# Kernel optimization log

Measured on AMD Instinct MI355X. Metric: run time of the kernel, lower is better.

## Reference

```python
import jax, jax.numpy as jnp
import numpy as np

BETA = 0.25
DECAY = 0.99
EPS = 1e-05
K = 1024        # num_codebook_vectors
D = 256         # latent_dim


def setup_inputs() -> dict:
    key = jax.random.key(0)
    k1, k2, k3 = jax.random.split(key, 3)
    return {
        "z": jax.random.normal(k1, (32, D, 32, 32), dtype=jnp.float32),
        "embedding": jax.random.normal(k2, (K, D), dtype=jnp.float32),
        "ema_cluster_size": jnp.zeros((K,), dtype=jnp.float32),
        "ema_w": jax.random.normal(k3, (K, D), dtype=jnp.float32),
    }


def reference(z, embedding, ema_cluster_size, ema_w):
    B, C, H, W = z.shape
    zp = jnp.transpose(z, (0, 2, 3, 1))            # [B,H,W,C]
    zf = zp.reshape(-1, C)                          # [N, D], N = B*H*W

    # squared L2 distances: ||z||^2 + ||e||^2 - 2 z e^T  -> [N, K]
    d = (jnp.sum(zf * zf, axis=1, keepdims=True)
         + jnp.sum(embedding * embedding, axis=1)
         - 2.0 * (zf @ embedding.T))
    idx = jnp.argmin(d, axis=1)                     # [N]

    # one-hot @ embedding == gather of codebook rows
    z_q = embedding[idx].reshape(zp.shape)          # [B,H,W,C]

    # EMA codebook update (training branch)
    counts = jnp.zeros((K,), dtype=zf.dtype).at[idx].add(1.0)   # encodings.sum(0)
    cs = ema_cluster_size * DECAY + (1.0 - DECAY) * counts
    n = jnp.sum(cs)
    cs = (cs + EPS) / (n + K * EPS) * n             # Laplace smoothing
    dw = jax.ops.segment_sum(zf, idx, num_segments=K)           # encodings.T @ zf
    new_ema_w = ema_w * DECAY + (1.0 - DECAY) * dw
    new_embedding = new_ema_w / cs[:, None]

    # commitment loss + straight-through estimator
    e_latent_loss = jnp.mean((jax.lax.stop_gradient(z_q) - zp) ** 2)
    loss = BETA * e_latent_loss
    z_q_st = zp + jax.lax.stop_gradient(z_q - zp)
    z_q_out = jnp.transpose(z_q_st, (0, 3, 1, 2))   # [B,C,H,W]

    return z_q_out, idx[:, None], loss, new_embedding, cs, new_ema_w
```

## Files before the change

### kernel.cpp

```cpp
#include <hip/hip_runtime.h>

typedef unsigned long long ull;
typedef __attribute__((ext_vector_type(8))) short bf16x8;
typedef __attribute__((ext_vector_type(4))) float f32x4;
typedef __attribute__((ext_vector_type(8))) unsigned short u16x8;

#define DECAY 0.99f
#define BETA 0.25f
#define EPSV 1e-5f
#define EPSGAP 0.0625f

#define Dd 256
#define Kk 1024
#define Nn 32768
#define ZELEM 8388608

__device__ __forceinline__ unsigned short f2bf(float f) {
    unsigned int x = __float_as_uint(f);
    x += 0x7FFFu + ((x >> 16) & 1u);
    return (unsigned short)(x >> 16);
}
__device__ __forceinline__ float bf2f(unsigned short b) {
    return __uint_as_float(((unsigned int)b) << 16);
}
__device__ __forceinline__ unsigned mono(unsigned b) {
    return b ^ (((int)b >> 31) | 0x80000000u);
}
__device__ __forceinline__ float unmono(unsigned m) {
    unsigned b = (m & 0x80000000u) ? (m ^ 0x80000000u) : ~m;
    return __uint_as_float(b);
}
__device__ __forceinline__ unsigned umin32(unsigned a, unsigned b) { return a < b ? a : b; }
__device__ __forceinline__ unsigned umax32(unsigned a, unsigned b) { return a > b ? a : b; }

__global__ __launch_bounds__(256) void prep_e_kernel(
        const float* __restrict__ emb, unsigned short* __restrict__ ehg,
        unsigned short* __restrict__ elg, float* __restrict__ esq,
        int* __restrict__ hist, int* __restrict__ flagcnt,
        float* __restrict__ loss_fix, float* __restrict__ nsum,
        const float* __restrict__ ema_cs, float* __restrict__ dwr, int nrep) {
    const int nsub = blockIdx.x;
    const int t = threadIdx.x;
    {
        const int per = nrep * 512;
        float4* dst = (float4*)(dwr + (size_t)nsub * per);
        const int n4 = per >> 2;
        for (int j = t; j < n4; j += 256) dst[j] = make_float4(0.f, 0.f, 0.f, 0.f);
    }
    if (nsub < 64) {
        if (t < 16) hist[nsub * 16 + t] = 0;
        if (nsub == 0 && t == 16) flagcnt[0] = 0;
        if (nsub == 0 && t == 17) loss_fix[0] = 0.0f;
        #pragma unroll
        for (int it = 0; it < 2; ++it) {
            const int item = it * 256 + t;
            const int kc = item >> 6, lane = item & 63;
            const int quad = lane >> 4, nl = lane & 15;
            const float* ep = emb + (size_t)(nsub * 16 + nl) * Dd + kc * 32 + quad * 8;
            const float4 a = *(const float4*)ep;
            const float4 b4 = *(const float4*)(ep + 4);
            const float v[8] = {a.x, a.y, a.z, a.w, b4.x, b4.y, b4.z, b4.w};
            u16x8 hi, lo;
            #pragma unroll
            for (int j = 0; j < 8; ++j) {
                const unsigned short h = f2bf(v[j]);
                hi[j] = h;
                lo[j] = f2bf(v[j] - bf2f(h));
            }
            const size_t off = ((size_t)(nsub * 8 + kc) * 64 + lane) * 8;
            *(u16x8*)&ehg[off] = hi;
            *(u16x8*)&elg[off] = lo;
        }
        {
            const int nl = t >> 4, seg = t & 15;
            const float* ep = emb + (size_t)(nsub * 16 + nl) * Dd + seg * 16;
            float s = 0.0f;
            #pragma unroll
            for (int j = 0; j < 4; ++j) {
                const float4 v4 = *(const float4*)(ep + j * 4);
                s += v4.x * v4.x + v4.y * v4.y + v4.z * v4.z + v4.w * v4.w;
            }
            #pragma unroll
            for (int d = 1; d < 16; d <<= 1) s += __shfl_xor(s, d);
            if (seg == 0) esq[nsub * 16 + nl] = s;
        }
    } else if (nsub == 64) {
        __shared__ float wred[4];
        const int w = t >> 6, lane = t & 63;
        float s = ema_cs[t] + ema_cs[t + 256] + ema_cs[t + 512] + ema_cs[t + 768];
        #pragma unroll
        for (int d = 32; d > 0; d >>= 1) s += __shfl_xor(s, d);
        if (lane == 0) wred[w] = s;
        __syncthreads();
        if (t == 0)
            nsum[0] = DECAY * (wred[0] + wred[1] + wred[2] + wred[3])
                      + (1.0f - DECAY) * (float)Nn;
    }
}

__global__ __launch_bounds__(256) void dist_kernel(
        const float* __restrict__ z, const unsigned short* __restrict__ ehg,
        const unsigned short* __restrict__ elg, const float* __restrict__ esq,
        const float* __restrict__ emb,
        float* __restrict__ zq, float* __restrict__ dwr, int repmask,
        int* __restrict__ idx_i, float* __restrict__ idx_f,
        int* __restrict__ hist, int* __restrict__ flagcnt,
        int* __restrict__ flaglist, float* __restrict__ flagval,
        float* __restrict__ loss_p) {
    __shared__ __align__(16) unsigned char smem[70656];
    __shared__ int kidx[64];
    unsigned short* zh = (unsigned short*)smem;
    unsigned short* zl = (unsigned short*)(smem + 32768);
    ull* mb   = (ull*)(smem + 65536);
    ull* ms   = (ull*)(smem + 67584);
    float* zsqp = (float*)(smem + 69632);
    float* eldsf = (float*)smem;

    const int t = threadIdx.x, w = t >> 6, L = t & 63;
    const int quad = L >> 4, lr = L & 15;
    const int m0 = blockIdx.x * 64;
    const int b = m0 >> 10, hw0 = m0 & 1023;

    {
        const int c0 = w * 64;
        const float* zp = z + (size_t)b * 262144 + hw0 + L;
        float s = 0.0f;
        #pragma unroll
        for (int cg = 0; cg < 8; ++cg) {
            float v[8];
            #pragma unroll
            for (int j = 0; j < 8; ++j)
                v[j] = zp[(size_t)(c0 + cg * 8 + j) * 1024];
            u16x8 hi, lo;
            #pragma unroll
            for (int j = 0; j < 8; ++j) {
                s = fmaf(v[j], v[j], s);
                const unsigned short h = f2bf(v[j]);
                hi[j] = h;
                lo[j] = f2bf(v[j] - bf2f(h));
            }
            const int chunk = ((c0 >> 3) + cg) ^ (L & 7);
            *(u16x8*)&zh[L * 256 + chunk * 8] = hi;
            *(u16x8*)&zl[L * 256 + chunk * 8] = lo;
        }
        zsqp[L * 4 + w] = s;
    }
    __syncthreads();

    const unsigned short* ehw = ehg + (size_t)(w * 1024 + L) * 8;
    const unsigned short* elw = elg + (size_t)(w * 1024 + L) * 8;

    unsigned bb[16], ss[16];
    #pragma unroll
    for (int i = 0; i < 16; ++i) { bb[i] = 0xFFFFFFFFu; ss[i] = 0xFFFFFFFFu; }

    bf16x8 Bh[2][2], Bl[2][2];
    #pragma unroll
    for (int ni = 0; ni < 2; ++ni) {
        Bh[0][ni] = *(const bf16x8*)(ehw + (size_t)ni * 4096);
        Bl[0][ni] = *(const bf16x8*)(elw + (size_t)ni * 4096);
    }
    bf16x8 Ah[2][4], Al[2][4];
    #pragma unroll
    for (int mi = 0; mi < 4; ++mi) {
        const int chunk = quad ^ (lr & 7);
        const int o = (mi * 16 + lr) * 256 + chunk * 8;
        Ah[0][mi] = *(const bf16x8*)&zh[o];
        Al[0][mi] = *(const bf16x8*)&zl[o];
    }

    for (int nt = 0; nt < 8; ++nt) {
        f32x4 acc[4][2];
        #pragma unroll
        for (int mi = 0; mi < 4; ++mi)
            #pragma unroll
            for (int ni = 0; ni < 2; ++ni) acc[mi][ni] = (f32x4){0.f, 0.f, 0.f, 0.f};

        #pragma unroll
        for (int kc = 0; kc < 8; ++kc) {
            const int cur = kc & 1, nxt = cur ^ 1;
            const int nkc = (kc + 1) & 7;
            const int nnt = (kc == 7) ? ((nt + 1) & 7) : nt;
            #pragma unroll
            for (int ni = 0; ni < 2; ++ni) {
                const size_t o = (size_t)nnt * 32768 + (size_t)ni * 4096 + (size_t)nkc * 512;
                Bh[nxt][ni] = *(const bf16x8*)(ehw + o);
                Bl[nxt][ni] = *(const bf16x8*)(elw + o);
            }
            #pragma unroll
            for (int mi = 0; mi < 4; ++mi) {
                const int chunk = (nkc * 4 + quad) ^ (lr & 7);
                const int o = (mi * 16 + lr) * 256 + chunk * 8;
                Ah[nxt][mi] = *(const bf16x8*)&zh[o];
                Al[nxt][mi] = *(const bf16x8*)&zl[o];
            }
            __builtin_amdgcn_s_setprio(1);
            #pragma unroll
            for (int mi = 0; mi < 4; ++mi)
                #pragma unroll
                for (int ni = 0; ni < 2; ++ni) {
                    acc[mi][ni] = __builtin_amdgcn_mfma_f32_16x16x32_bf16(Ah[cur][mi], Bh[cur][ni], acc[mi][ni], 0, 0, 0);
                    acc[mi][ni] = __builtin_amdgcn_mfma_f32_16x16x32_bf16(Ah[cur][mi], Bl[cur][ni], acc[mi][ni], 0, 0, 0);
                    acc[mi][ni] = __builtin_amdgcn_mfma_f32_16x16x32_bf16(Al[cur][mi], Bh[cur][ni], acc[mi][ni], 0, 0, 0);
                }
            __builtin_amdgcn_s_setprio(0);
        }
        const int q0 = nt * 8 + w * 2;
        const float e0b = esq[q0 * 16 + lr] + 512.0f;
        const float e1b = esq[(q0 + 1) * 16 + lr] + 512.0f;
        #pragma unroll
        for (int mi = 0; mi < 4; ++mi)
            #pragma unroll
            for (int reg = 0; reg < 4; ++reg) {
                const int i = mi * 4 + reg;
                #pragma unroll
                for (int ni = 0; ni < 2; ++ni) {
                    const float val = fmaf(-2.0f, acc[mi][ni][reg], ni ? e1b : e0b);
                    const unsigned pk = (__float_as_uint(val) & 0xFFFFFFC0u) | (unsigned)(q0 + ni);
                    const unsigned mx = umax32(bb[i], pk);
                    bb[i] = umin32(bb[i], pk);
                    ss[i] = umin32(ss[i], mx);
                }
            }
    }

    #pragma unroll
    for (int mi = 0; mi < 4; ++mi)
        #pragma unroll
        for (int reg = 0; reg < 4; ++reg) {
            const int i = mi * 4 + reg;
            ull b2 = ((ull)(bb[i] & 0xFFFFFFC0u) << 14) | (ull)((bb[i] & 63u) * 16 + lr);
            ull s2 = ((ull)(ss[i] & 0xFFFFFFC0u) << 14) | (ull)((ss[i] & 63u) * 16 + lr);
            #pragma unroll
            for (int d = 1; d < 16; d <<= 1) {
                const ull ob = __shfl_xor(b2, d);
                const ull os = __shfl_xor(s2, d);
                const ull mx = ob < b2 ? b2 : ob;
                b2 = ob < b2 ? ob : b2;
                const ull ns = os < s2 ? os : s2;
                s2 = mx < ns ? mx : ns;
            }
            if (lr == 0) {
                const int row = mi * 16 + quad * 4 + reg;
                mb[w * 64 + row] = b2;
                ms[w * 64 + row] = s2;
            }
        }
    __syncthreads();

    if (t < 64) {
        ull b2 = mb[t], s2 = ms[t];
        #pragma unroll
        for (int ww = 1; ww < 4; ++ww) {
            const ull ob = mb[ww * 64 + t], os = ms[ww * 64 + t];
            const ull mx = ob < b2 ? b2 : ob;
            b2 = ob < b2 ? ob : b2;
            const ull ns = os < s2 ? os : s2;
            s2 = mx < ns ? mx : ns;
        }
        const int k = (int)(b2 & 16383ull);
        const float v1 = __uint_as_float((unsigned)(b2 >> 14)) - 512.0f;
        const float v2 = __uint_as_float((unsigned)(s2 >> 14)) - 512.0f;
        idx_i[m0 + t] = k;
        idx_f[m0 + t] = (float)k;
        kidx[t] = k;
        atomicAdd(&hist[k], 1);
        if (v2 - v1 < EPSGAP) {
            const int pos = atomicAdd(flagcnt, 1);
            flaglist[pos] = m0 + t;
            flagval[pos] = v1;
        }
        float lp = v1 + zsqp[t * 4] + zsqp[t * 4 + 1] + zsqp[t * 4 + 2] + zsqp[t * 4 + 3];
        #pragma unroll
        for (int d = 32; d > 0; d >>= 1) lp += __shfl_down(lp, d);
        if (t == 0) loss_p[blockIdx.x] = lp;
    }
    __syncthreads();

    for (int pr = w; pr < 64; pr += 4) {
        const float* er = emb + (size_t)kidx[pr] * Dd;
        #pragma unroll
        for (int g = 0; g < 4; ++g)
            eldsf[pr * 257 + g * 64 + L] = er[g * 64 + L];
    }
    __syncthreads();

    {
        const int g = t & 15;
        const int cl = t >> 4;
        float* zqb = zq + (size_t)b * 262144 + hw0 + g * 4;
        #pragma unroll
        for (int pass = 0; pass < 16; ++pass) {
            const int c = pass * 16 + cl;
            float4 v;
            v.x = eldsf[(g * 4 + 0) * 257 + c];
            v.y = eldsf[(g * 4 + 1) * 257 + c];
            v.z = eldsf[(g * 4 + 2) * 257 + c];
            v.w = eldsf[(g * 4 + 3) * 257 + c];
            *(float4*)(zqb + (size_t)c * 1024) = v;
        }
    }

    {
        const int c = t;
        const float* zcol = z + (size_t)b * 262144 + (size_t)c * 1024 + hw0;
        float* dwb = dwr + (size_t)(blockIdx.x & repmask) * (Kk * Dd);
        #pragma unroll 4
        for (int p = 0; p < 64; ++p) {
            atomicAdd(&dwb[(size_t)kidx[p] * Dd + c], zcol[p]);
        }
    }
}

__global__ __launch_bounds__(256) void fixup_kernel(
        const float* __restrict__ z, const float* __restrict__ emb,
        const float* __restrict__ esq, const int* __restrict__ flagcnt,
        const int* __restrict__ flaglist, const float* __restrict__ flagval,
        int* __restrict__ idx_i, float* __restrict__ idx_f,
        int* __restrict__ hist, float* __restrict__ loss_fix,
        float* __restrict__ zq, float* __restrict__ dw) {
    __shared__ float zrow[256];
    __shared__ ull red[256];
    __shared__ int s_pair[2];
    const int t = threadIdx.x;
    const int total = flagcnt[0];
    for (int fi = blockIdx.x; fi < total; fi += 512) {
        const int n = flaglist[fi];
        const int b = n >> 10, hw = n & 1023;
        __syncthreads();
        zrow[t] = z[(size_t)b * 262144 + (size_t)t * 1024 + hw];
        __syncthreads();
        ull best = ~0ull;
        #pragma unroll
        for (int kc = 0; kc < 4; ++kc) {
            const int k = t * 4 + kc;
            const float* ep = emb + (size_t)k * Dd;
            float dot = 0.0f;
            #pragma unroll 8
            for (int c4 = 0; c4 < 64; ++c4) {
                const float4 e4 = *(const float4*)(ep + c4 * 4);
                const float4 z4 = *(const float4*)&zrow[c4 * 4];
                dot = fmaf(z4.x, e4.x, dot);
                dot = fmaf(z4.y, e4.y, dot);
                dot = fmaf(z4.z, e4.z, dot);
                dot = fmaf(z4.w, e4.w, dot);
            }
            const float val = esq[k] - 2.0f * dot;
            const ull pk = ((ull)mono(__float_as_uint(val)) << 32) | (unsigned)k;
            if (pk < best) best = pk;
        }
        red[t] = best;
        __syncthreads();
        for (int s = 128; s > 0; s >>= 1) {
            if (t < s) { if (red[t + s] < red[t]) red[t] = red[t + s]; }
            __syncthreads();
        }
        if (t == 0) {
            const int knew = (int)(unsigned)(red[0] & 0xFFFFFFFFull);
            const float vnew = unmono((unsigned)(red[0] >> 32));
            const int kold = idx_i[n];
            s_pair[0] = kold;
            s_pair[1] = knew;
            if (knew != kold) {
                idx_i[n] = knew;
                idx_f[n] = (float)knew;
                atomicSub(&hist[kold], 1);
                atomicAdd(&hist[knew], 1);
            }
            atomicAdd(loss_fix, vnew - flagval[fi]);
        }
        __syncthreads();
        const int kold = s_pair[0], knew = s_pair[1];
        if (knew != kold) {
            const float zv = zrow[t];
            atomicAdd(&dw[(size_t)kold * Dd + t], -zv);
            atomicAdd(&dw[(size_t)knew * Dd + t], zv);
            zq[(size_t)b * 262144 + (size_t)t * 1024 + hw] = emb[(size_t)knew * Dd + t];
        }
    }
}

__global__ __launch_bounds__(256) void finalize2_kernel(
        const float* __restrict__ ema_w, const float* __restrict__ dwr,
        int nrep, const int* __restrict__ hist,
        const float* __restrict__ ema_cs, const float* __restrict__ nsum,
        const float* __restrict__ loss_p, const float* __restrict__ loss_fix,
        float* __restrict__ cs_out, float* __restrict__ loss_out,
        float* __restrict__ new_emb_out, float* __restrict__ new_ema_w_out) {
    const int k = blockIdx.x;
    const int t = threadIdx.x;
    const float n = nsum[0];
    const float csr = ema_cs[k] * DECAY + (1.0f - DECAY) * (float)hist[k];
    const float cs = (csr + EPSV) / (n + (float)Kk * EPSV) * n;
    if (t == 0) cs_out[k] = cs;
    const int i = k * 256 + t;
    float s = 0.0f;
    for (int r = 0; r < nrep; ++r) s += dwr[(size_t)r * (Kk * Dd) + i];
    const float nw = ema_w[i] * DECAY + (1.0f - DECAY) * s;
    new_ema_w_out[i] = nw;
    new_emb_out[i]   = nw / cs;
    if (k == 0) {
        __shared__ float wred[4];
        const int w = t >> 6, lane = t & 63;
        float r2 = loss_p[t] + loss_p[t + 256];
        #pragma unroll
        for (int d = 32; d > 0; d >>= 1) r2 += __shfl_xor(r2, d);
        if (lane == 0) wred[w] = r2;
        __syncthreads();
        if (t == 0)
            loss_out[0] = BETA * (wred[0] + wred[1] + wred[2] + wred[3]
                                  + loss_fix[0]) / (float)ZELEM;
    }
}

extern "C" void kernel_launch(void* const* d_in, const int* in_sizes, int n_in,
                              void* d_out, int out_size, void* d_ws, size_t ws_size,
                              hipStream_t stream) {
    const float* z      = (const float*)d_in[0];
    const float* emb    = (const float*)d_in[1];
    const float* ema_cs = (const float*)d_in[2];
    const float* ema_w  = (const float*)d_in[3];

    float* out = (float*)d_out;
    float* zq_out        = out;
    float* idx_out_f     = out + 8388608;
    float* loss_out      = out + 8421376;
    float* new_emb_out   = out + 8421377;
    float* cs_out        = out + 8683521;
    float* new_ema_w_out = out + 8684545;

    int*   idx_i    = (int*)d_ws;
    int*   flagcnt  = idx_i + 32768;
    float* loss_fix = (float*)(flagcnt + 16);
    int*   flaglist = (int*)(loss_fix + 16);
    float* flagval  = (float*)(flaglist + 32768);
    int*   hist     = (int*)(flagval + 32768);
    float* esq      = (float*)(hist + 1024);
    float* loss_p   = esq + 1024;
    float* nsum     = loss_p + 512;
    unsigned short* ehg = (unsigned short*)(nsum + 16);
    unsigned short* elg = ehg + 262144;
    size_t dwr_off = ((size_t)((char*)(elg + 262144) - (char*)d_ws) + 255) & ~(size_t)255;
    float* dwr = (float*)((char*)d_ws + dwr_off);
    const size_t repbytes = (size_t)Kk * Dd * 4;
    size_t rem = (ws_size > dwr_off) ? ws_size - dwr_off : 0;
    int nrep = 1;
    while (nrep < 8 && (size_t)(nrep * 2) * repbytes <= rem) nrep <<= 1;

    prep_e_kernel<<<512, 256, 0, stream>>>(emb, ehg, elg, esq, hist, flagcnt,
                                           loss_fix, nsum, ema_cs, dwr, nrep);
    dist_kernel<<<Nn / 64, 256, 0, stream>>>(z, ehg, elg, esq, emb, zq_out,
                                             dwr, nrep - 1, idx_i, idx_out_f,
                                             hist, flagcnt, flaglist, flagval,
                                             loss_p);
    fixup_kernel<<<512, 256, 0, stream>>>(z, emb, esq, flagcnt, flaglist,
                                          flagval, idx_i, idx_out_f, hist,
                                          loss_fix, zq_out, dwr);
    finalize2_kernel<<<Kk, 256, 0, stream>>>(ema_w, dwr, nrep, hist, ema_cs,
                                             nsum, loss_p, loss_fix, cs_out,
                                             loss_out, new_emb_out,
                                             new_ema_w_out);
}
```

Before: 231.6 us.

## Track top-3 candidates to split fixup into cheap two-candidate and full rescans

The distance kernel now keeps the three best candidates per row instead of two. Near-tie rows whose third candidate is far enough away go to a new list that the fixup kernel resolves with two exact fp32 dot products. Only rows with a close third candidate still get the full 1024-code rescan. The change aims to cut fixup cost, at the price of extra min/max and shuffle work in the hot distance kernel's per-tile selection and reduction.

```diff
diff --git a/kernel.cpp b/kernel.cpp
--- a/kernel.cpp
+++ b/kernel.cpp
@@ -9,6 +9,7 @@
 #define BETA 0.25f
 #define EPSV 1e-5f
 #define EPSGAP 0.0625f
+#define THR3 0.03125f
 
 #define Dd 256
 #define Kk 1024
@@ -32,6 +33,8 @@
 }
 __device__ __forceinline__ unsigned umin32(unsigned a, unsigned b) { return a < b ? a : b; }
 __device__ __forceinline__ unsigned umax32(unsigned a, unsigned b) { return a > b ? a : b; }
+__device__ __forceinline__ ull umin64(ull a, ull b) { return a < b ? a : b; }
+__device__ __forceinline__ ull umax64(ull a, ull b) { return a > b ? a : b; }
 
 __global__ __launch_bounds__(256) void prep_e_kernel(
         const float* __restrict__ emb, unsigned short* __restrict__ ehg,
@@ -51,6 +54,7 @@
         if (t < 16) hist[nsub * 16 + t] = 0;
         if (nsub == 0 && t == 16) flagcnt[0] = 0;
         if (nsub == 0 && t == 17) loss_fix[0] = 0.0f;
+        if (nsub == 0 && t == 18) flagcnt[1] = 0;
         #pragma unroll
         for (int it = 0; it < 2; ++it) {
             const int item = it * 256 + t;
@@ -105,15 +109,17 @@
         float* __restrict__ zq, float* __restrict__ dwr, int repmask,
         int* __restrict__ idx_i, float* __restrict__ idx_f,
         int* __restrict__ hist, int* __restrict__ flagcnt,
-        int* __restrict__ flaglist, float* __restrict__ flagval,
-        float* __restrict__ loss_p) {
-    __shared__ __align__(16) unsigned char smem[70656];
+        int* __restrict__ listA, int* __restrict__ kkA,
+        float* __restrict__ valA, int* __restrict__ listB,
+        float* __restrict__ valB, float* __restrict__ loss_p) {
+    __shared__ __align__(16) unsigned char smem[72704];
     __shared__ int kidx[64];
     unsigned short* zh = (unsigned short*)smem;
     unsigned short* zl = (unsigned short*)(smem + 32768);
     ull* mb   = (ull*)(smem + 65536);
     ull* ms   = (ull*)(smem + 67584);
     float* zsqp = (float*)(smem + 69632);
+    ull* mt   = (ull*)(smem + 70656);
     float* eldsf = (float*)smem;
 
     const int t = threadIdx.x, w = t >> 6, L = t & 63;
@@ -150,9 +156,9 @@
     const unsigned short* ehw = ehg + (size_t)(w * 1024 + L) * 8;
     const unsigned short* elw = elg + (size_t)(w * 1024 + L) * 8;
 
-    unsigned bb[16], ss[16];
+    unsigned bb[16], ss[16], tt[16];
     #pragma unroll
-    for (int i = 0; i < 16; ++i) { bb[i] = 0xFFFFFFFFu; ss[i] = 0xFFFFFFFFu; }
+    for (int i = 0; i < 16; ++i) { bb[i] = 0xFFFFFFFFu; ss[i] = 0xFFFFFFFFu; tt[i] = 0xFFFFFFFFu; }
 
     bf16x8 Bh[2][2], Bl[2][2];
     #pragma unroll
@@ -217,9 +223,10 @@
                 for (int ni = 0; ni < 2; ++ni) {
                     const float val = fmaf(-2.0f, acc[mi][ni][reg], ni ? e1b : e0b);
                     const unsigned pk = (__float_as_uint(val) & 0xFFFFFFC0u) | (unsigned)(q0 + ni);
-                    const unsigned mx = umax32(bb[i], pk);
-                    bb[i] = umin32(bb[i], pk);
-                    ss[i] = umin32(ss[i], mx);
+                    const unsigned m1 = umin32(bb[i], pk), M1 = umax32(bb[i], pk);
+                    const unsigned m2 = umin32(ss[i], M1), M2 = umax32(ss[i], M1);
+                    const unsigned m3 = umin32(tt[i], M2);
+                    bb[i] = m1; ss[i] = m2; tt[i] = m3;
                 }
             }
     }
@@ -231,44 +238,60 @@
             const int i = mi * 4 + reg;
             ull b2 = ((ull)(bb[i] & 0xFFFFFFC0u) << 14) | (ull)((bb[i] & 63u) * 16 + lr);
             ull s2 = ((ull)(ss[i] & 0xFFFFFFC0u) << 14) | (ull)((ss[i] & 63u) * 16 + lr);
+            ull t2 = ((ull)(tt[i] & 0xFFFFFFC0u) << 14) | (ull)((tt[i] & 63u) * 16 + lr);
             #pragma unroll
             for (int d = 1; d < 16; d <<= 1) {
                 const ull ob = __shfl_xor(b2, d);
                 const ull os = __shfl_xor(s2, d);
-                const ull mx = ob < b2 ? b2 : ob;
-                b2 = ob < b2 ? ob : b2;
-                const ull ns = os < s2 ? os : s2;
-                s2 = mx < ns ? mx : ns;
+                const ull ot = __shfl_xor(t2, d);
+                const ull x1 = umin64(b2, ob), y1 = umax64(b2, ob);
+                const ull x2 = umin64(s2, os), y2 = umax64(s2, os);
+                const ull c2 = umin64(y1, x2);
+                const ull t1 = umax64(y1, x2);
+                const ull c3 = umin64(t1, umin64(y2, umin64(t2, ot)));
+                b2 = x1; s2 = c2; t2 = c3;
             }
             if (lr == 0) {
                 const int row = mi * 16 + quad * 4 + reg;
                 mb[w * 64 + row] = b2;
                 ms[w * 64 + row] = s2;
+                mt[w * 64 + row] = t2;
             }
         }
     __syncthreads();
 
     if (t < 64) {
-        ull b2 = mb[t], s2 = ms[t];
+        ull b2 = mb[t], s2 = ms[t], t2 = mt[t];
         #pragma unroll
         for (int ww = 1; ww < 4; ++ww) {
-            const ull ob = mb[ww * 64 + t], os = ms[ww * 64 + t];
-            const ull mx = ob < b2 ? b2 : ob;
-            b2 = ob < b2 ? ob : b2;
-            const ull ns = os < s2 ? os : s2;
-            s2 = mx < ns ? mx : ns;
-        }
-        const int k = (int)(b2 & 16383ull);
+            const ull ob = mb[ww * 64 + t], os = ms[ww * 64 + t], ot = mt[ww * 64 + t];
+            const ull x1 = umin64(b2, ob), y1 = umax64(b2, ob);
+            const ull x2 = umin64(s2, os), y2 = umax64(s2, os);
+            const ull c2 = umin64(y1, x2);
+            const ull t1 = umax64(y1, x2);
+            const ull c3 = umin64(t1, umin64(y2, umin64(t2, ot)));
+            b2 = x1; s2 = c2; t2 = c3;
+        }
+        const int k1 = (int)(b2 & 16383ull);
+        const int k2 = (int)(s2 & 16383ull);
         const float v1 = __uint_as_float((unsigned)(b2 >> 14)) - 512.0f;
         const float v2 = __uint_as_float((unsigned)(s2 >> 14)) - 512.0f;
-        idx_i[m0 + t] = k;
-        idx_f[m0 + t] = (float)k;
-        kidx[t] = k;
-        atomicAdd(&hist[k], 1);
+        const float v3 = __uint_as_float((unsigned)(t2 >> 14)) - 512.0f;
+        idx_i[m0 + t] = k1;
+        idx_f[m0 + t] = (float)k1;
+        kidx[t] = k1;
+        atomicAdd(&hist[k1], 1);
         if (v2 - v1 < EPSGAP) {
-            const int pos = atomicAdd(flagcnt, 1);
-            flaglist[pos] = m0 + t;
-            flagval[pos] = v1;
+            if (v3 - v1 < THR3) {
+                const int pos = atomicAdd(&flagcnt[1], 1);
+                listB[pos] = m0 + t;
+                valB[pos] = v1;
+            } else {
+                const int pos = atomicAdd(&flagcnt[0], 1);
+                listA[pos] = m0 + t;
+                kkA[pos] = k1 | (k2 << 16);
+                valA[pos] = v1;
+            }
         }
         float lp = v1 + zsqp[t * 4] + zsqp[t * 4 + 1] + zsqp[t * 4 + 2] + zsqp[t * 4 + 3];
         #pragma unroll
@@ -315,17 +338,69 @@
 __global__ __launch_bounds__(256) void fixup_kernel(
         const float* __restrict__ z, const float* __restrict__ emb,
         const float* __restrict__ esq, const int* __restrict__ flagcnt,
-        const int* __restrict__ flaglist, const float* __restrict__ flagval,
+        const int* __restrict__ listA, const int* __restrict__ kkA,
+        const float* __restrict__ valA, const int* __restrict__ listB,
+        const float* __restrict__ valB,
         int* __restrict__ idx_i, float* __restrict__ idx_f,
         int* __restrict__ hist, float* __restrict__ loss_fix,
         float* __restrict__ zq, float* __restrict__ dw) {
     __shared__ float zrow[256];
+    __shared__ float red1[4], red2[4];
     __shared__ ull red[256];
     __shared__ int s_pair[2];
     const int t = threadIdx.x;
-    const int total = flagcnt[0];
-    for (int fi = blockIdx.x; fi < total; fi += 512) {
-        const int n = flaglist[fi];
+    const int w = t >> 6, lane = t & 63;
+
+    const int totalA = flagcnt[0];
+    for (int fi = blockIdx.x; fi < totalA; fi += 512) {
+        const int n = listA[fi];
+        const int b = n >> 10, hw = n & 1023;
+        const int kk = kkA[fi];
+        const int k1 = kk & 0xFFFF, k2 = kk >> 16;
+        __syncthreads();
+        zrow[t] = z[(size_t)b * 262144 + (size_t)t * 1024 + hw];
+        __syncthreads();
+        const float zv = zrow[t];
+        float c1 = zv * emb[(size_t)k1 * Dd + t];
+        float c2 = zv * emb[(size_t)k2 * Dd + t];
+        #pragma unroll
+        for (int d = 32; d > 0; d >>= 1) {
+            c1 += __shfl_xor(c1, d);
+            c2 += __shfl_xor(c2, d);
+        }
+        if (lane == 0) { red1[w] = c1; red2[w] = c2; }
+        __syncthreads();
+        if (t == 0) {
+            const float d1 = esq[k1] - 2.0f * (red1[0] + red1[1] + red1[2] + red1[3]);
+            const float d2 = esq[k2] - 2.0f * (red2[0] + red2[1] + red2[2] + red2[3]);
+            const ull p1 = ((ull)mono(__float_as_uint(d1)) << 32) | (unsigned)k1;
+            const ull p2 = ((ull)mono(__float_as_uint(d2)) << 32) | (unsigned)k2;
+            const ull pb = p1 < p2 ? p1 : p2;
+            const int knew = (int)(unsigned)(pb & 0xFFFFFFFFull);
+            const float vnew = unmono((unsigned)(pb >> 32));
+            const int kold = idx_i[n];
+            s_pair[0] = kold;
+            s_pair[1] = knew;
+            if (knew != kold) {
+                idx_i[n] = knew;
+                idx_f[n] = (float)knew;
+                atomicSub(&hist[kold], 1);
+                atomicAdd(&hist[knew], 1);
+            }
+            atomicAdd(loss_fix, vnew - valA[fi]);
+        }
+        __syncthreads();
+        const int kold = s_pair[0], knew = s_pair[1];
+        if (knew != kold) {
+            atomicAdd(&dw[(size_t)kold * Dd + t], -zv);
+            atomicAdd(&dw[(size_t)knew * Dd + t], zv);
+            zq[(size_t)b * 262144 + (size_t)t * 1024 + hw] = emb[(size_t)knew * Dd + t];
+        }
+    }
+
+    const int totalB = flagcnt[1];
+    for (int fi = blockIdx.x; fi < totalB; fi += 512) {
+        const int n = listB[fi];
         const int b = n >> 10, hw = n & 1023;
         __syncthreads();
         zrow[t] = z[(size_t)b * 262144 + (size_t)t * 1024 + hw];
@@ -367,7 +442,7 @@
                 atomicSub(&hist[kold], 1);
                 atomicAdd(&hist[knew], 1);
             }
-            atomicAdd(loss_fix, vnew - flagval[fi]);
+            atomicAdd(loss_fix, vnew - valB[fi]);
         }
         __syncthreads();
         const int kold = s_pair[0], knew = s_pair[1];
@@ -432,9 +507,12 @@
     int*   idx_i    = (int*)d_ws;
     int*   flagcnt  = idx_i + 32768;
     float* loss_fix = (float*)(flagcnt + 16);
-    int*   flaglist = (int*)(loss_fix + 16);
-    float* flagval  = (float*)(flaglist + 32768);
-    int*   hist     = (int*)(flagval + 32768);
+    int*   listA    = (int*)(loss_fix + 16);
+    float* valA     = (float*)(listA + 32768);
+    int*   kkA      = (int*)(valA + 32768);
+    int*   listB    = kkA + 32768;
+    float* valB     = (float*)(listB + 32768);
+    int*   hist     = (int*)(valB + 32768);
     float* esq      = (float*)(hist + 1024);
     float* loss_p   = esq + 1024;
     float* nsum     = loss_p + 512;
@@ -451,11 +529,11 @@
                                            loss_fix, nsum, ema_cs, dwr, nrep);
     dist_kernel<<<Nn / 64, 256, 0, stream>>>(z, ehg, elg, esq, emb, zq_out,
                                              dwr, nrep - 1, idx_i, idx_out_f,
-                                             hist, flagcnt, flaglist, flagval,
-                                             loss_p);
-    fixup_kernel<<<512, 256, 0, stream>>>(z, emb, esq, flagcnt, flaglist,
-                                          flagval, idx_i, idx_out_f, hist,
-                                          loss_fix, zq_out, dwr);
+                                             hist, flagcnt, listA, kkA, valA,
+                                             listB, valB, loss_p);
+    fixup_kernel<<<512, 256, 0, stream>>>(z, emb, esq, flagcnt, listA, kkA,
+                                          valA, listB, valB, idx_i, idx_out_f,
+                                          hist, loss_fix, zq_out, dwr);
     finalize2_kernel<<<Kk, 256, 0, stream>>>(ema_w, dwr, nrep, hist, ema_cs,
                                              nsum, loss_p, loss_fix, cs_out,
                                              loss_out, new_emb_out,
```

Result: faster. 213.2 us (-7.9%).
